# Kernel tuning notes

Measured on AMD Instinct MI355X. Metric: run time of the kernel, lower is better.

The kernel has to match this reference:

```python
import jax, jax.numpy as jnp
import numpy as np

DECAY = 0.9        # membrane leak per step
THRESH = 1.0       # spike threshold
SLOPE = 4.0        # fast-sigmoid surrogate slope
W_SCALE = 0.01     # weight init scale to keep dynamics sane


def _spike_fn(v):
    # Heaviside forward, fast-sigmoid surrogate backward (straight-through).
    s = jax.nn.sigmoid(SLOPE * (v - THRESH))
    h = (v > THRESH).astype(v.dtype)
    return jax.lax.stop_gradient(h - s) + s


def setup_inputs() -> dict:
    key = jax.random.key(0)
    ks = jax.random.split(key, 6)
    T, B, NE, NI = 64, 32, 4096, 1024
    return {
        "ext_exc": jax.random.normal(ks[0], (T, B, NE), dtype=jnp.float32),
        "ext_inh": jax.random.normal(ks[1], (T, B, NI), dtype=jnp.float32),
        "W_ee": jax.random.normal(ks[2], (NE, NE), dtype=jnp.float32) * W_SCALE,
        "W_ei": jax.random.normal(ks[3], (NI, NE), dtype=jnp.float32) * W_SCALE,
        "W_ie": jax.random.normal(ks[4], (NE, NI), dtype=jnp.float32) * W_SCALE,
        "W_ii": jax.random.normal(ks[5], (NI, NI), dtype=jnp.float32) * W_SCALE,
        "time_steps": 64,
    }


def reference(ext_exc, ext_inh, W_ee, W_ei, W_ie, W_ii, time_steps):
    B, NE = ext_exc.shape[1], ext_exc.shape[2]
    NI = ext_inh.shape[2]
    dt = ext_exc.dtype
    v_e = jnp.zeros((B, NE), dt)
    v_i = jnp.zeros((B, NI), dt)
    s_e = jnp.zeros((B, NE), dt)
    s_i = jnp.zeros((B, NI), dt)

    def step(carry, xs):
        v_e, v_i, s_e, s_i = carry
        ie_ext, ii_ext = xs
        # recurrent currents from PREVIOUS step spikes (matches current_spikes semantics)
        i_e = ie_ext + s_e @ W_ee.T + s_i @ W_ie.T
        i_i = ii_ext + s_e @ W_ei.T + s_i @ W_ii.T
        # LIF update: leak + integrate, spike, hard reset
        v_e = v_e * DECAY + i_e
        v_i = v_i * DECAY + i_i
        ns_e = _spike_fn(v_e)
        ns_i = _spike_fn(v_i)
        v_e = v_e * (1.0 - ns_e)
        v_i = v_i * (1.0 - ns_i)
        return (v_e, v_i, ns_e, ns_i), (ns_e, ns_i)

    xs = (ext_exc[:time_steps], ext_inh[:time_steps])
    _, (hist_e, hist_i) = jax.lax.scan(step, (v_e, v_i, s_e, s_i), xs)
    # spike_history as one array: [T, B, NE+NI] (exc then inh populations)
    return jnp.concatenate([hist_e, hist_i], axis=-1)
```

## Files before the change

### kernel.cpp

```cpp
#include <hip/hip_runtime.h>


#define NE 4096
#define NI 1024
#define NN 5120
#define HN 2560
#define BB 32
#define JH 16
#define CHUNK 160

template <int KR>
__global__ __launch_bounds__(256) void mv_kernel(
    const float* __restrict__ W_ee, const float* __restrict__ W_ei,
    const float* __restrict__ W_ie, const float* __restrict__ W_ii,
    const float* __restrict__ sd,
    double* __restrict__ partial)
{
    __shared__ float s_l[BB][CHUNK];
    const int t  = threadIdx.x;
    const int tn = t & 127;
    const int jh = (t >> 7) << 4;
    const int nA = blockIdx.x * 128 + tn;
    const int nB = nA + HN;
    const int kb0 = blockIdx.y * KR;

    double accA[JH], accB[JH];
#pragma unroll
    for (int j = 0; j < JH; ++j) { accA[j] = 0.0; accB[j] = 0.0; }

    const float* __restrict__ rEA = W_ee + (size_t)nA * NE;
    const float* __restrict__ rIA = W_ie + (size_t)nA * NI;
    const float* __restrict__ rEB = (nB < NE) ? (W_ee + (size_t)nB * NE)
                                              : (W_ei + (size_t)(nB - NE) * NE);
    const float* __restrict__ rIB = (nB < NE) ? (W_ie + (size_t)nB * NI)
                                              : (W_ii + (size_t)(nB - NE) * NI);

    for (int pass = 0; pass < KR / CHUNK; ++pass) {
        const int kb = kb0 + pass * CHUNK;

        if (pass) __syncthreads();
        for (int f = t; f < BB * (CHUNK / 4); f += 256) {
            const int j = f / (CHUNK / 4);
            const int q = f - j * (CHUNK / 4);
            *reinterpret_cast<float4*>(&s_l[j][q * 4]) =
                *reinterpret_cast<const float4*>(sd + (size_t)j * NN + kb + q * 4);
        }
        __syncthreads();

        int aEnd = NE - kb;
        if (aEnd < 0) aEnd = 0;
        if (aEnd > CHUNK) aEnd = CHUNK;

        for (int kk = 0; kk < aEnd; kk += 4) {
            const float4 wa = *reinterpret_cast<const float4*>(rEA + kb + kk);
            const float4 wb = *reinterpret_cast<const float4*>(rEB + kb + kk);
            const double wa0 = (double)wa.x, wa1 = (double)wa.y,
                         wa2 = (double)wa.z, wa3 = (double)wa.w;
            const double wb0 = (double)wb.x, wb1 = (double)wb.y,
                         wb2 = (double)wb.z, wb3 = (double)wb.w;
#pragma unroll
            for (int j = 0; j < JH; ++j) {
                const float4 sv = *reinterpret_cast<const float4*>(&s_l[jh + j][kk]);
                const double s0 = (double)sv.x, s1 = (double)sv.y,
                             s2 = (double)sv.z, s3 = (double)sv.w;
                accA[j] += wa0 * s0 + wa1 * s1 + wa2 * s2 + wa3 * s3;
                accB[j] += wb0 * s0 + wb1 * s1 + wb2 * s2 + wb3 * s3;
            }
        }
        for (int kk = aEnd; kk < CHUNK; kk += 4) {
            const int ki = kb + kk - NE;
            const float4 wa = *reinterpret_cast<const float4*>(rIA + ki);
            const float4 wb = *reinterpret_cast<const float4*>(rIB + ki);
            const double wa0 = (double)wa.x, wa1 = (double)wa.y,
                         wa2 = (double)wa.z, wa3 = (double)wa.w;
            const double wb0 = (double)wb.x, wb1 = (double)wb.y,
                         wb2 = (double)wb.z, wb3 = (double)wb.w;
#pragma unroll
            for (int j = 0; j < JH; ++j) {
                const float4 sv = *reinterpret_cast<const float4*>(&s_l[jh + j][kk]);
                const double s0 = (double)sv.x, s1 = (double)sv.y,
                             s2 = (double)sv.z, s3 = (double)sv.w;
                accA[j] += wa0 * s0 + wa1 * s1 + wa2 * s2 + wa3 * s3;
                accB[j] += wb0 * s0 + wb1 * s1 + wb2 * s2 + wb3 * s3;
            }
        }
    }

#pragma unroll
    for (int j = 0; j < JH; ++j) {
        const size_t base = ((size_t)blockIdx.y * BB + jh + j) * NN;
        partial[base + nA] = accA[j];
        partial[base + nB] = accB[j];
    }
}

template <int G>
__global__ __launch_bounds__(256) void upd_kernel(
    const float* __restrict__ ext_exc,
    const float* __restrict__ ext_inh,
    const double* __restrict__ partial,
    double* __restrict__ v,
    float* __restrict__ sd,
    float* __restrict__ out,
    int t)
{
    const int idx = blockIdx.x * 256 + threadIdx.x;
    const int b = idx / NN;
    const int n = idx - b * NN;

    const float ext = (n < NE)
        ? ext_exc[((size_t)t * BB + b) * NE + n]
        : ext_inh[((size_t)t * BB + b) * NI + (n - NE)];

    double acc = (double)ext;
#pragma unroll
    for (int g = 0; g < G; ++g)
        acc += partial[((size_t)g * BB + b) * NN + n];

    const double vv = v[idx] * 0.9 + acc;
    const double sp = (vv > 1.0) ? 1.0 : 0.0;
    out[(size_t)t * BB * NN + idx] = (float)sp;
    v[idx] = vv * (1.0 - sp);
    sd[idx] = (float)sp;
}

extern "C" void kernel_launch(void* const* d_in, const int* in_sizes, int n_in,
                              void* d_out, int out_size, void* d_ws, size_t ws_size,
                              hipStream_t stream) {
    const float* ext_exc = (const float*)d_in[0];
    const float* ext_inh = (const float*)d_in[1];
    const float* W_ee = (const float*)d_in[2];
    const float* W_ei = (const float*)d_in[3];
    const float* W_ie = (const float*)d_in[4];
    const float* W_ii = (const float*)d_in[5];
    float* out = (float*)d_out;

    const int T = in_sizes[0] / (BB * NE);

    const size_t SN = (size_t)BB * NN;
    double* v = (double*)d_ws;
    float* sd = (float*)(v + SN);
    double* partial = (double*)(sd + SN);
    const size_t stateBytes = SN * 12;

    int G = 32;
    while (G > 8 && stateBytes + (size_t)G * SN * sizeof(double) > ws_size) G >>= 1;

    hipMemsetAsync(d_ws, 0, stateBytes, stream);

    for (int t = 0; t < T; ++t) {
        switch (G) {
            case 32:
                mv_kernel<160> <<<dim3(HN/128, 32), 256, 0, stream>>>(W_ee, W_ei, W_ie, W_ii, sd, partial);
                upd_kernel<32><<<(int)(SN/256), 256, 0, stream>>>(ext_exc, ext_inh, partial, v, sd, out, t);
                break;
            case 16:
                mv_kernel<320> <<<dim3(HN/128, 16), 256, 0, stream>>>(W_ee, W_ei, W_ie, W_ii, sd, partial);
                upd_kernel<16><<<(int)(SN/256), 256, 0, stream>>>(ext_exc, ext_inh, partial, v, sd, out, t);
                break;
            default:
                mv_kernel<640> <<<dim3(HN/128, 8), 256, 0, stream>>>(W_ee, W_ei, W_ie, W_ii, sd, partial);
                upd_kernel<8> <<<(int)(SN/256), 256, 0, stream>>>(ext_exc, ext_inh, partial, v, sd, out, t);
                break;
        }
    }
}
```

Before: 4.678 ms.

## Pack spikes into per-neuron batch bitmasks and skip zero-spike columns in matvec

Adds a pack kernel that turns each step's spike output into a 32-bit batch mask per presynaptic neuron. The matvec kernel then reads the masks with wave-uniform readfirstlane instead of staging float spikes through shared memory. It skips groups of four columns where no batch in its 8-row slice spiked and replaces multiply-adds with conditional fp64 adds. Blocks shrink to 64 neurons with 8 batches per wave slice, the weight loads are software-prefetched, and one extra small launch is added per time step.

Result: slower. 6.951 ms (+48.6%).

```diff
diff --git a/kernel.cpp b/kernel.cpp
--- a/kernel.cpp
+++ b/kernel.cpp
@@ -6,27 +6,35 @@
 #define NN 5120
 #define HN 2560
 #define BB 32
-#define JH 16
-#define CHUNK 160
+
+__global__ __launch_bounds__(256) void pack_kernel(
+    const float* __restrict__ out_t, unsigned* __restrict__ mask)
+{
+    const int n = blockIdx.x * 256 + threadIdx.x;
+    unsigned m = 0;
+#pragma unroll
+    for (int b = 0; b < BB; ++b)
+        m |= (out_t[(size_t)b * NN + n] > 0.5f ? 1u : 0u) << b;
+    mask[n] = m;
+}
 
 template <int KR>
 __global__ __launch_bounds__(256) void mv_kernel(
     const float* __restrict__ W_ee, const float* __restrict__ W_ei,
     const float* __restrict__ W_ie, const float* __restrict__ W_ii,
-    const float* __restrict__ sd,
+    const unsigned* __restrict__ mask,
     double* __restrict__ partial)
 {
-    __shared__ float s_l[BB][CHUNK];
     const int t  = threadIdx.x;
-    const int tn = t & 127;
-    const int jh = (t >> 7) << 4;
-    const int nA = blockIdx.x * 128 + tn;
+    const int tn = t & 63;
+    const int jh = __builtin_amdgcn_readfirstlane((t >> 6) << 3);
+    const int nA = blockIdx.x * 64 + tn;
     const int nB = nA + HN;
-    const int kb0 = blockIdx.y * KR;
+    const int kb = blockIdx.y * KR;
 
-    double accA[JH], accB[JH];
+    double accA[8], accB[8];
 #pragma unroll
-    for (int j = 0; j < JH; ++j) { accA[j] = 0.0; accB[j] = 0.0; }
+    for (int j = 0; j < 8; ++j) { accA[j] = 0.0; accB[j] = 0.0; }
 
     const float* __restrict__ rEA = W_ee + (size_t)nA * NE;
     const float* __restrict__ rIA = W_ie + (size_t)nA * NI;
@@ -35,59 +43,50 @@
     const float* __restrict__ rIB = (nB < NE) ? (W_ie + (size_t)nB * NI)
                                               : (W_ii + (size_t)(nB - NE) * NI);
 
-    for (int pass = 0; pass < KR / CHUNK; ++pass) {
-        const int kb = kb0 + pass * CHUNK;
+    int aEnd = NE - kb;
+    if (aEnd < 0) aEnd = 0;
+    if (aEnd > KR) aEnd = KR;
 
-        if (pass) __syncthreads();
-        for (int f = t; f < BB * (CHUNK / 4); f += 256) {
-            const int j = f / (CHUNK / 4);
-            const int q = f - j * (CHUNK / 4);
-            *reinterpret_cast<float4*>(&s_l[j][q * 4]) =
-                *reinterpret_cast<const float4*>(sd + (size_t)j * NN + kb + q * 4);
-        }
-        __syncthreads();
+    auto run = [&](const float* __restrict__ pA, const float* __restrict__ pB,
+                   const unsigned* __restrict__ pM, int len) {
+        if (len <= 0) return;
+        float4 wa = *reinterpret_cast<const float4*>(pA);
+        float4 wb = *reinterpret_cast<const float4*>(pB);
+        uint4  mq = *reinterpret_cast<const uint4*>(pM);
+        for (int kk = 0; kk < len; kk += 4) {
+            const float4 cwa = wa, cwb = wb;
+            const uint4  cmq = mq;
+            if (kk + 4 < len) {
+                wa = *reinterpret_cast<const float4*>(pA + kk + 4);
+                wb = *reinterpret_cast<const float4*>(pB + kk + 4);
+                mq = *reinterpret_cast<const uint4*>(pM + kk + 4);
+            }
+            const unsigned m0 = (__builtin_amdgcn_readfirstlane(cmq.x) >> jh) & 0xFFu;
+            const unsigned m1 = (__builtin_amdgcn_readfirstlane(cmq.y) >> jh) & 0xFFu;
+            const unsigned m2 = (__builtin_amdgcn_readfirstlane(cmq.z) >> jh) & 0xFFu;
+            const unsigned m3 = (__builtin_amdgcn_readfirstlane(cmq.w) >> jh) & 0xFFu;
+            if ((m0 | m1 | m2 | m3) == 0u) continue;
 
-        int aEnd = NE - kb;
-        if (aEnd < 0) aEnd = 0;
-        if (aEnd > CHUNK) aEnd = CHUNK;
-
-        for (int kk = 0; kk < aEnd; kk += 4) {
-            const float4 wa = *reinterpret_cast<const float4*>(rEA + kb + kk);
-            const float4 wb = *reinterpret_cast<const float4*>(rEB + kb + kk);
-            const double wa0 = (double)wa.x, wa1 = (double)wa.y,
-                         wa2 = (double)wa.z, wa3 = (double)wa.w;
-            const double wb0 = (double)wb.x, wb1 = (double)wb.y,
-                         wb2 = (double)wb.z, wb3 = (double)wb.w;
+            const double wa0 = (double)cwa.x, wa1 = (double)cwa.y,
+                         wa2 = (double)cwa.z, wa3 = (double)cwa.w;
+            const double wb0 = (double)cwb.x, wb1 = (double)cwb.y,
+                         wb2 = (double)cwb.z, wb3 = (double)cwb.w;
 #pragma unroll
-            for (int j = 0; j < JH; ++j) {
-                const float4 sv = *reinterpret_cast<const float4*>(&s_l[jh + j][kk]);
-                const double s0 = (double)sv.x, s1 = (double)sv.y,
-                             s2 = (double)sv.z, s3 = (double)sv.w;
-                accA[j] += wa0 * s0 + wa1 * s1 + wa2 * s2 + wa3 * s3;
-                accB[j] += wb0 * s0 + wb1 * s1 + wb2 * s2 + wb3 * s3;
+            for (int j = 0; j < 8; ++j) {
+                if (m0 & (1u << j)) { accA[j] += wa0; accB[j] += wb0; }
+                if (m1 & (1u << j)) { accA[j] += wa1; accB[j] += wb1; }
+                if (m2 & (1u << j)) { accA[j] += wa2; accB[j] += wb2; }
+                if (m3 & (1u << j)) { accA[j] += wa3; accB[j] += wb3; }
             }
         }
-        for (int kk = aEnd; kk < CHUNK; kk += 4) {
-            const int ki = kb + kk - NE;
-            const float4 wa = *reinterpret_cast<const float4*>(rIA + ki);
-            const float4 wb = *reinterpret_cast<const float4*>(rIB + ki);
-            const double wa0 = (double)wa.x, wa1 = (double)wa.y,
-                         wa2 = (double)wa.z, wa3 = (double)wa.w;
-            const double wb0 = (double)wb.x, wb1 = (double)wb.y,
-                         wb2 = (double)wb.z, wb3 = (double)wb.w;
-#pragma unroll
-            for (int j = 0; j < JH; ++j) {
-                const float4 sv = *reinterpret_cast<const float4*>(&s_l[jh + j][kk]);
-                const double s0 = (double)sv.x, s1 = (double)sv.y,
-                             s2 = (double)sv.z, s3 = (double)sv.w;
-                accA[j] += wa0 * s0 + wa1 * s1 + wa2 * s2 + wa3 * s3;
-                accB[j] += wb0 * s0 + wb1 * s1 + wb2 * s2 + wb3 * s3;
-            }
-        }
-    }
+    };
+
+    run(rEA + kb, rEB + kb, mask + kb, aEnd);
+    run(rIA + (kb + aEnd - NE), rIB + (kb + aEnd - NE), mask + kb + aEnd,
+        KR - aEnd);
 
 #pragma unroll
-    for (int j = 0; j < JH; ++j) {
+    for (int j = 0; j < 8; ++j) {
         const size_t base = ((size_t)blockIdx.y * BB + jh + j) * NN;
         partial[base + nA] = accA[j];
         partial[base + nB] = accB[j];
@@ -100,7 +99,6 @@
     const float* __restrict__ ext_inh,
     const double* __restrict__ partial,
     double* __restrict__ v,
-    float* __restrict__ sd,
     float* __restrict__ out,
     int t)
 {
@@ -121,7 +119,6 @@
     const double sp = (vv > 1.0) ? 1.0 : 0.0;
     out[(size_t)t * BB * NN + idx] = (float)sp;
     v[idx] = vv * (1.0 - sp);
-    sd[idx] = (float)sp;
 }
 
 extern "C" void kernel_launch(void* const* d_in, const int* in_sizes, int n_in,
@@ -139,9 +136,9 @@
 
     const size_t SN = (size_t)BB * NN;
     double* v = (double*)d_ws;
-    float* sd = (float*)(v + SN);
-    double* partial = (double*)(sd + SN);
-    const size_t stateBytes = SN * 12;
+    unsigned* mask = (unsigned*)(v + SN);
+    double* partial = (double*)((char*)d_ws + SN * 8 + NN * 4);
+    const size_t stateBytes = SN * 8 + NN * 4;
 
     int G = 32;
     while (G > 8 && stateBytes + (size_t)G * SN * sizeof(double) > ws_size) G >>= 1;
@@ -151,17 +148,18 @@
     for (int t = 0; t < T; ++t) {
         switch (G) {
             case 32:
-                mv_kernel<160> <<<dim3(HN/128, 32), 256, 0, stream>>>(W_ee, W_ei, W_ie, W_ii, sd, partial);
-                upd_kernel<32><<<(int)(SN/256), 256, 0, stream>>>(ext_exc, ext_inh, partial, v, sd, out, t);
+                mv_kernel<160> <<<dim3(HN/64, 32), 256, 0, stream>>>(W_ee, W_ei, W_ie, W_ii, mask, partial);
+                upd_kernel<32><<<(int)(SN/256), 256, 0, stream>>>(ext_exc, ext_inh, partial, v, out, t);
                 break;
             case 16:
-                mv_kernel<320> <<<dim3(HN/128, 16), 256, 0, stream>>>(W_ee, W_ei, W_ie, W_ii, sd, partial);
-                upd_kernel<16><<<(int)(SN/256), 256, 0, stream>>>(ext_exc, ext_inh, partial, v, sd, out, t);
+                mv_kernel<320> <<<dim3(HN/64, 16), 256, 0, stream>>>(W_ee, W_ei, W_ie, W_ii, mask, partial);
+                upd_kernel<16><<<(int)(SN/256), 256, 0, stream>>>(ext_exc, ext_inh, partial, v, out, t);
                 break;
             default:
-                mv_kernel<640> <<<dim3(HN/128, 8), 256, 0, stream>>>(W_ee, W_ei, W_ie, W_ii, sd, partial);
-                upd_kernel<8> <<<(int)(SN/256), 256, 0, stream>>>(ext_exc, ext_inh, partial, v, sd, out, t);
+                mv_kernel<640> <<<dim3(HN/64, 8), 256, 0, stream>>>(W_ee, W_ei, W_ie, W_ii, mask, partial);
+                upd_kernel<8> <<<(int)(SN/256), 256, 0, stream>>>(ext_exc, ext_inh, partial, v, out, t);
                 break;
         }
+        pack_kernel<<<NN/256, 256, 0, stream>>>(out + (size_t)t * SN, mask);
     }
 }
```
